# Kernel optimization log

Measured on AMD Instinct MI355X. Metric: run time of the kernel, lower is better.

## Reference

```python
import jax, jax.numpy as jnp
import numpy as np
import math

DIM = 512
HEADS = 8
DIM_HEAD = 64
SCALE = math.sqrt(DIM_HEAD)
EPS = 1e-12


def rms_norm(x, g):
    # F.normalize(x, dim=1) * g * sqrt(dim); x: [B, C, H, W], g: [C]
    inv = jax.lax.rsqrt(jnp.sum(x * x, axis=1, keepdims=True) + EPS)
    return x * inv * g[None, :, None, None] * jnp.asarray(math.sqrt(x.shape[1]), x.dtype)


def setup_inputs() -> dict:
    key = jax.random.key(0)
    k1, k2, k3 = jax.random.split(key, 3)
    B, H, W = 8, 64, 64
    hidden = HEADS * DIM_HEAD
    x = jax.random.normal(k1, (B, DIM, H, W), dtype=jnp.float32)
    w_qkv = jax.random.normal(k2, (3 * hidden, DIM), dtype=jnp.float32) * (1.0 / math.sqrt(DIM))
    w_out = jax.random.normal(k3, (DIM, hidden), dtype=jnp.float32) * (1.0 / math.sqrt(hidden))
    b_out = jnp.zeros((DIM,), dtype=jnp.float32)
    g1 = jnp.ones((DIM,), dtype=jnp.float32)
    g2 = jnp.ones((DIM,), dtype=jnp.float32)
    return {"x": x, "g1": g1, "w_qkv": w_qkv, "w_out": w_out, "b_out": b_out, "g2": g2}


def reference(x, g1, w_qkv, w_out, b_out, g2):
    B, C, H, W = x.shape
    n = H * W
    xn = rms_norm(x, g1)
    # 1x1 conv == channel matmul: [B, 3*hidden, H, W]
    qkv = jnp.einsum('bchw,oc->bohw', xn, w_qkv)
    q, k, v = jnp.split(qkv, 3, axis=1)
    # b (h c) x y -> b h c n
    def to_heads(t):
        return t.reshape(B, HEADS, DIM_HEAD, n)
    q, k, v = to_heads(q), to_heads(k), to_heads(v)
    q = jax.nn.softmax(q, axis=2) / SCALE   # softmax over channel dim d
    k = jax.nn.softmax(k, axis=3)           # softmax over spatial dim n
    context = jnp.einsum('bhdn,bhen->bhde', k, v)   # [B, H, d, e]
    out = jnp.einsum('bhde,bhdn->bhen', context, q) # [B, H, e, n]
    out = out.reshape(B, HEADS * DIM_HEAD, H, W)
    out = jnp.einsum('bchw,oc->bohw', out, w_out) + b_out[None, :, None, None]
    return rms_norm(out, g2)
```

## Files before the change

kernel.cpp:

```cpp
#include <hip/hip_runtime.h>


typedef unsigned short u16;
typedef __attribute__((ext_vector_type(8))) short short8;
typedef __attribute__((ext_vector_type(4))) short short4_t;
typedef __attribute__((ext_vector_type(4))) float f32x4;

static constexpr size_t XN_B = (size_t)512 * 4096;
static constexpr size_t KV_B = (size_t)1024 * 4096;
static constexpr float SQRT512 = 22.62741699796952f;

typedef const __attribute__((address_space(1))) unsigned int gu32;
typedef __attribute__((address_space(3))) unsigned int lu32;

__device__ __forceinline__ float b2f(u16 u){
  union { unsigned u; float f; } x; x.u = ((unsigned)u) << 16; return x.f;
}
__device__ __forceinline__ u16 f2b(float f){
  union { float f; unsigned u; } x; x.f = f;
  unsigned r = x.u + 0x7FFFu + ((x.u >> 16) & 1u);
  return (u16)(r >> 16);
}
__device__ __forceinline__ void gl16(const u16* g, u16* l){
  __builtin_amdgcn_global_load_lds((gu32*)g, (lu32*)l, 16, 0, 0);
}

__global__ __launch_bounds__(256)
void kprep(const float* __restrict__ wqkv, const float* __restrict__ wout,
           const float* __restrict__ g1, u16* __restrict__ dq, u16* __restrict__ dw,
           const float* __restrict__ x, u16* __restrict__ xnT,
           float* __restrict__ sden){
  __shared__ u16 lt[32][514];
  __shared__ float red[256];
  __shared__ float invs[32];
  int bid = blockIdx.x;
  int t = threadIdx.x;
  if (bid < 1024){
    if (bid < 16) sden[bid * 256 + t] = 0.f;
    size_t i = ((size_t)bid * 256 + t) * 4;
    short4_t o;
    if (i < (size_t)786432){
      f32x4 v = *(const f32x4*)(wqkv + i);
      int c = (int)(i & 511);
      #pragma unroll
      for (int j = 0; j < 4; j++) o[j] = (short)f2b(v[j] * g1[c + j] * SQRT512);
      *(short4_t*)(dq + i) = o;
    } else {
      size_t off = i - 786432;
      f32x4 v = *(const f32x4*)(wout + off);
      #pragma unroll
      for (int j = 0; j < 4; j++) o[j] = (short)f2b(v[j]);
      *(short4_t*)(dw + off) = o;
    }
    return;
  }
  int pg0 = (bid - 1024) * 32;
  int b = pg0 >> 12, p0 = pg0 & 4095;
  int px = t & 31, chunk = t >> 5;
  const float* xp = x + (size_t)b * XN_B + p0 + px;
  float s = 0.f;
  #pragma unroll 4
  for (int c = chunk * 64; c < chunk * 64 + 64; ++c){
    float v = xp[(size_t)c * 4096];
    lt[px][c] = f2b(v);
    s += v * v;
  }
  red[t] = s;
  __syncthreads();
  if (chunk == 0){
    float tt = red[px] + red[px + 32] + red[px + 64] + red[px + 96]
             + red[px + 128] + red[px + 160] + red[px + 192] + red[px + 224];
    invs[px] = rsqrtf(tt + 1e-12f);
  }
  __syncthreads();
  int px2 = t >> 3, c0 = (t & 7) * 8;
  float iv = invs[px2];
  u16* dst = xnT + (size_t)(pg0 + px2) * 512;
  #pragma unroll
  for (int j = 0; j < 8; j++){
    int c = c0 + j * 64;
    short8 o;
    #pragma unroll
    for (int e = 0; e < 8; e++) o[e] = (short)f2b(b2f(lt[px2][c + e]) * iv);
    *(short8*)(dst + c) = o;
  }
}

template<int ADD_BIAS, int SMAX>
__global__ __launch_bounds__(512)
void gemm_big(const u16* __restrict__ Ab, long astr, int lda,
              const u16* __restrict__ Bb, long bstr, int ldb,
              u16* __restrict__ Cb, long cstr, int ldc,
              const float* __restrict__ bias)
{
  constexpr int NT = 16;
  const u16* A  = Ab + (size_t)blockIdx.z * astr;
  const u16* BT = Bb + (size_t)blockIdx.z * bstr;
  u16* C = Cb + (size_t)blockIdx.z * cstr;
  const int m0 = blockIdx.y * 256, n0 = blockIdx.x * 256;
  __shared__ u16 As[2][256 * 32];
  __shared__ u16 Bs[2][256 * 32];
  const int tid = threadIdx.x;
  const int lane = tid & 63, wid = tid >> 6;
  const int wr = (wid >> 2) * 128, wc = (wid & 3) * 64;
  const int fr = lane & 15, fq = lane >> 4;
  const int srow = tid >> 2;
  const int sslot = tid & 3;
  f32x4 acc[8][4] = {};

  auto STAGE = [&](int s, int t){
    const int k0 = t * 32;
    #pragma unroll
    for (int r = 0; r < 2; r++){
      int row = r * 128 + srow;
      int gj = (sslot ^ ((row >> 1) & 3)) * 8;
      gl16(A  + (size_t)(m0 + row) * lda + k0 + gj, &As[s][0] + r * 4096 + tid * 8);
      gl16(BT + (size_t)(n0 + row) * ldb + k0 + gj, &Bs[s][0] + r * 4096 + tid * 8);
    }
  };

  STAGE(0, 0);
  int cur = 0;
  for (int t = 0; t < NT; t++){
    if (t + 1 < NT){
      STAGE(cur ^ 1, t + 1);
      asm volatile("s_waitcnt vmcnt(4)" ::: "memory");
    } else {
      asm volatile("s_waitcnt vmcnt(0)" ::: "memory");
    }
    __builtin_amdgcn_s_barrier();
    __builtin_amdgcn_sched_barrier(0);
    short8 a[8], b[4];
    #pragma unroll
    for (int i = 0; i < 8; i++){
      int ra = wr + i * 16 + fr;
      a[i] = *(const short8*)(&As[cur][0] + ra * 32 + ((fq ^ ((ra >> 1) & 3)) * 8));
    }
    #pragma unroll
    for (int j = 0; j < 4; j++){
      int rb = wc + j * 16 + fr;
      b[j] = *(const short8*)(&Bs[cur][0] + rb * 32 + ((fq ^ ((rb >> 1) & 3)) * 8));
    }
    __builtin_amdgcn_s_setprio(1);
    #pragma unroll
    for (int i = 0; i < 8; i++)
      #pragma unroll
      for (int j = 0; j < 4; j++)
        acc[i][j] = __builtin_amdgcn_mfma_f32_16x16x32_bf16(a[i], b[j], acc[i][j], 0, 0, 0);
    __builtin_amdgcn_s_setprio(0);
    __builtin_amdgcn_sched_barrier(0);
    __builtin_amdgcn_s_barrier();
    cur ^= 1;
  }

  if constexpr (SMAX){
    #pragma unroll
    for (int i = 0; i < 8; i++)
      #pragma unroll
      for (int e = 0; e < 4; e++){
        float mx = fmaxf(fmaxf(acc[i][0][e], acc[i][1][e]),
                         fmaxf(acc[i][2][e], acc[i][3][e]));
        mx = fmaxf(mx, __shfl_xor(mx, 1));
        mx = fmaxf(mx, __shfl_xor(mx, 2));
        mx = fmaxf(mx, __shfl_xor(mx, 4));
        mx = fmaxf(mx, __shfl_xor(mx, 8));
        float p0 = __expf(acc[i][0][e] - mx);
        float p1 = __expf(acc[i][1][e] - mx);
        float p2 = __expf(acc[i][2][e] - mx);
        float p3 = __expf(acc[i][3][e] - mx);
        float s = p0 + p1 + p2 + p3;
        s += __shfl_xor(s, 1);
        s += __shfl_xor(s, 2);
        s += __shfl_xor(s, 4);
        s += __shfl_xor(s, 8);
        float r = 1.f / (s * 8.0f);
        acc[i][0][e] = p0 * r; acc[i][1][e] = p1 * r;
        acc[i][2][e] = p2 * r; acc[i][3][e] = p3 * r;
      }
  }
  #pragma unroll
  for (int i = 0; i < 8; i++)
    #pragma unroll
    for (int j = 0; j < 4; j++)
      #pragma unroll
      for (int e = 0; e < 4; e++){
        int row = m0 + wr + i * 16 + fq * 4 + e;
        int col = n0 + wc + j * 16 + fr;
        float v = acc[i][j][e];
        if constexpr (ADD_BIAS) v += bias[col];
        C[(size_t)row * ldc + col] = f2b(v);
      }
}

__global__ __launch_bounds__(256)
void gemm_kv(const u16* __restrict__ Wkv, const u16* __restrict__ xnT,
             u16* __restrict__ kvb)
{
  constexpr int NT = 8;
  const int z = blockIdx.z;
  const u16* A  = Wkv;
  const u16* BT = xnT + (size_t)z * XN_B;
  u16* C = kvb + (size_t)z * KV_B;
  const int m0 = blockIdx.y * 128, n0 = blockIdx.x * 128;
  __shared__ u16 As[2][128 * 64];
  __shared__ u16 Bs[2][128 * 64];
  const int tid = threadIdx.x;
  const int srow0 = tid >> 3;
  const int schunk = tid & 7;
  const int lane = tid & 63, wid = tid >> 6;
  const int wr = (wid >> 1) * 64, wc = (wid & 1) * 64;
  const int fr = lane & 15, fq = lane >> 4;
  f32x4 acc[4][4] = {};

  auto STAGE = [&](int s, int t){
    const int k0 = t * 64;
    #pragma unroll
    for (int r = 0; r < 4; r++){
      int row = r * 32 + srow0;
      int gj = (schunk ^ (row & 7)) * 8;
      gl16(A  + (size_t)(m0 + row) * 512 + k0 + gj, &As[s][0] + r * 2048 + tid * 8);
      gl16(BT + (size_t)(n0 + row) * 512 + k0 + gj, &Bs[s][0] + r * 2048 + tid * 8);
    }
  };

  STAGE(0, 0);
  int cur = 0;
  for (int t = 0; t < NT; t++){
    if (t + 1 < NT){
      STAGE(cur ^ 1, t + 1);
      asm volatile("s_waitcnt vmcnt(8)" ::: "memory");
    } else {
      asm volatile("s_waitcnt vmcnt(0)" ::: "memory");
    }
    __builtin_amdgcn_s_barrier();
    __builtin_amdgcn_sched_barrier(0);
    #pragma unroll
    for (int ks = 0; ks < 2; ks++){
      short8 a[4], b[4];
      #pragma unroll
      for (int i = 0; i < 4; i++){
        int ra = wr + i * 16 + fr;
        a[i] = *(const short8*)(&As[cur][0] + ra * 64 + ((ks * 4 + fq) ^ (ra & 7)) * 8);
        int rb = wc + i * 16 + fr;
        b[i] = *(const short8*)(&Bs[cur][0] + rb * 64 + ((ks * 4 + fq) ^ (rb & 7)) * 8);
      }
      #pragma unroll
      for (int i = 0; i < 4; i++)
        #pragma unroll
        for (int j = 0; j < 4; j++)
          acc[i][j] = __builtin_amdgcn_mfma_f32_16x16x32_bf16(a[i], b[j], acc[i][j], 0, 0, 0);
    }
    __builtin_amdgcn_sched_barrier(0);
    __builtin_amdgcn_s_barrier();
    cur ^= 1;
  }

  #pragma unroll
  for (int i = 0; i < 4; i++)
    #pragma unroll
    for (int j = 0; j < 4; j++)
      #pragma unroll
      for (int e = 0; e < 4; e++){
        int row = m0 + wr + i * 16 + fq * 4 + e;
        int col = n0 + wc + j * 16 + fr;
        C[(size_t)row * 4096 + col] = f2b(acc[i][j][e]);
      }
}

__global__ __launch_bounds__(256)
void gemm_ctx(const u16* __restrict__ kv, float* __restrict__ P,
              float* __restrict__ sden)
{
  constexpr int K = 512;
  const int z = blockIdx.z;
  const int tid = threadIdx.x;
  const int ar = tid >> 2, ac = (tid & 3) * 8;
  int bh = z >> 3, sp = z & 7, b = bh >> 3, h = bh & 7;
  const u16* A  = kv + (size_t)b * KV_B + (size_t)(h * 64) * 4096 + sp * 512;
  const u16* BT = kv + (size_t)b * KV_B + (size_t)(512 + h * 64) * 4096 + sp * 512;
  __shared__ u16 As[64 * 40];
  __shared__ u16 Bs[64 * 40];
  const int wid = tid >> 6, lane = tid & 63;
  const int wr = (wid >> 1) * 32, wc = (wid & 1) * 32;
  const int lr = lane & 15, kb = lane >> 4;
  f32x4 acc[2][2] = {};
  float ssum = 0.f;
  for (int k0 = 0; k0 < K; k0 += 32){
    short8 av = *(const short8*)(A + (size_t)ar * 4096 + k0 + ac);
    short8 ao;
    #pragma unroll
    for (int e = 0; e < 8; e++){
      float ev = __expf(b2f((u16)av[e]));
      ao[e] = (short)f2b(ev);
      ssum += ev;
    }
    *(short8*)(As + ar * 40 + ac) = ao;
    *(short8*)(Bs + ar * 40 + ac) = *(const short8*)(BT + (size_t)ar * 4096 + k0 + ac);
    __syncthreads();
    short8 a0 = *(const short8*)(As + (wr +      lr) * 40 + kb * 8);
    short8 a1 = *(const short8*)(As + (wr + 16 + lr) * 40 + kb * 8);
    short8 b0 = *(const short8*)(Bs + (wc +      lr) * 40 + kb * 8);
    short8 b1 = *(const short8*)(Bs + (wc + 16 + lr) * 40 + kb * 8);
    acc[0][0] = __builtin_amdgcn_mfma_f32_16x16x32_bf16(a0, b0, acc[0][0], 0, 0, 0);
    acc[0][1] = __builtin_amdgcn_mfma_f32_16x16x32_bf16(a0, b1, acc[0][1], 0, 0, 0);
    acc[1][0] = __builtin_amdgcn_mfma_f32_16x16x32_bf16(a1, b0, acc[1][0], 0, 0, 0);
    acc[1][1] = __builtin_amdgcn_mfma_f32_16x16x32_bf16(a1, b1, acc[1][1], 0, 0, 0);
    __syncthreads();
  }
  ssum += __shfl_xor(ssum, 1);
  ssum += __shfl_xor(ssum, 2);
  if ((tid & 3) == 0) atomicAdd(sden + b * 512 + h * 64 + ar, ssum);
  #pragma unroll
  for (int mi = 0; mi < 2; mi++)
    #pragma unroll
    for (int ni = 0; ni < 2; ni++)
      #pragma unroll
      for (int j = 0; j < 4; j++){
        int row = wr + mi * 16 + kb * 4 + j;
        int col = wc + ni * 16 + lr;
        P[(size_t)z * 4096 + (size_t)row * 64 + col] = acc[mi][ni][j];
      }
}

__global__ __launch_bounds__(256)
void kctxw(const float* __restrict__ P, const float* __restrict__ sden,
           const u16* __restrict__ woutbf, u16* __restrict__ M)
{
  const int z = blockIdx.z;
  const int b = z >> 3, h = z & 7;
  const int m0 = blockIdx.y * 64;
  const int tid = threadIdx.x;
  __shared__ u16 As[64 * 72];
  __shared__ u16 Bs[64 * 72];
  {
    int r = tid >> 2, c0 = (tid & 3) * 16;
    const u16* wsrc = woutbf + (size_t)(m0 + r) * 512 + h * 64 + c0;
    *(short8*)(As + r * 72 + c0)     = *(const short8*)(wsrc);
    *(short8*)(As + r * 72 + c0 + 8) = *(const short8*)(wsrc + 8);
    float rs = 1.f / sden[b * 512 + h * 64 + r];
    const float* p = P + (size_t)z * 32768 + (size_t)r * 64 + c0;
    #pragma unroll
    for (int e = 0; e < 16; e++){
      float s = 0.f;
      #pragma unroll
      for (int sp = 0; sp < 8; sp++) s += p[e + sp * 4096];
      Bs[r * 72 + c0 + e] = f2b(s * rs);
    }
  }
  __syncthreads();
  const int wid = tid >> 6, lane = tid & 63;
  const int wr = (wid >> 1) * 32, wc = (wid & 1) * 32;
  const int lr = lane & 15, kb = lane >> 4;
  f32x4 acc[2][2] = {};
  #pragma unroll
  for (int k0 = 0; k0 < 64; k0 += 32){
    short8 a0 = *(const short8*)(As + (wr +      lr) * 72 + k0 + kb * 8);
    short8 a1 = *(const short8*)(As + (wr + 16 + lr) * 72 + k0 + kb * 8);
    short8 b0 = *(const short8*)(Bs + (wc +      lr) * 72 + k0 + kb * 8);
    short8 b1 = *(const short8*)(Bs + (wc + 16 + lr) * 72 + k0 + kb * 8);
    acc[0][0] = __builtin_amdgcn_mfma_f32_16x16x32_bf16(a0, b0, acc[0][0], 0, 0, 0);
    acc[0][1] = __builtin_amdgcn_mfma_f32_16x16x32_bf16(a0, b1, acc[0][1], 0, 0, 0);
    acc[1][0] = __builtin_amdgcn_mfma_f32_16x16x32_bf16(a1, b0, acc[1][0], 0, 0, 0);
    acc[1][1] = __builtin_amdgcn_mfma_f32_16x16x32_bf16(a1, b1, acc[1][1], 0, 0, 0);
  }
  #pragma unroll
  for (int mi = 0; mi < 2; mi++)
    #pragma unroll
    for (int ni = 0; ni < 2; ni++)
      #pragma unroll
      for (int j = 0; j < 4; j++){
        int row = m0 + wr + mi * 16 + kb * 4 + j;
        int col = wc + ni * 16 + lr;
        M[(size_t)b * 262144 + (size_t)row * 512 + h * 64 + col] = f2b(acc[mi][ni][j]);
      }
}

__global__ __launch_bounds__(256)
void krms2(const u16* __restrict__ o2, const float* __restrict__ g,
           float* __restrict__ out){
  __shared__ u16 lt[32][514];
  __shared__ float invs[32];
  __shared__ float gl[512];
  int t = threadIdx.x;
  int pg0 = blockIdx.x * 32;
  int b = pg0 >> 12, p0 = pg0 & 4095;
  gl[t] = g[t] * SQRT512;
  gl[t + 256] = g[t + 256] * SQRT512;
  int px2 = t >> 3, c0 = (t & 7) * 8;
  const u16* src = o2 + (size_t)(pg0 + px2) * 512;
  float s = 0.f;
  #pragma unroll
  for (int j = 0; j < 8; j++){
    int c = c0 + j * 64;
    short8 v = *(const short8*)(src + c);
    *(short8*)&lt[px2][c] = v;
    #pragma unroll
    for (int e = 0; e < 8; e++){ float f = b2f((u16)v[e]); s += f * f; }
  }
  s += __shfl_xor(s, 1); s += __shfl_xor(s, 2); s += __shfl_xor(s, 4);
  if ((t & 7) == 0) invs[px2] = rsqrtf(s + 1e-12f);
  __syncthreads();
  int c2 = t >> 2, pxc = (t & 3) * 8;
  float ivv[8];
  #pragma unroll
  for (int e = 0; e < 8; e++) ivv[e] = invs[pxc + e];
  #pragma unroll
  for (int pass = 0; pass < 8; pass++){
    int c = c2 + pass * 64;
    float gf = gl[c];
    float* dst = out + ((size_t)(b * 512 + c)) * 4096 + p0 + pxc;
    #pragma unroll
    for (int q = 0; q < 2; q++){
      f32x4 o;
      #pragma unroll
      for (int e = 0; e < 4; e++){
        int pp = q * 4 + e;
        o[e] = b2f(lt[pxc + pp][c]) * ivv[pp] * gf;
      }
      *(f32x4*)(dst + q * 4) = o;
    }
  }
}

extern "C" void kernel_launch(void* const* d_in, const int* in_sizes, int n_in,
                              void* d_out, int out_size, void* d_ws, size_t ws_size,
                              hipStream_t stream)
{
  (void)in_sizes; (void)n_in; (void)out_size; (void)ws_size;
  const float* x    = (const float*)d_in[0];
  const float* g1   = (const float*)d_in[1];
  const float* wqkv = (const float*)d_in[2];
  const float* wout = (const float*)d_in[3];
  const float* bout = (const float*)d_in[4];
  const float* g2   = (const float*)d_in[5];
  float* out = (float*)d_out;
  char* ws = (char*)d_ws;

  u16*   xnT   = (u16*)(ws);
  float* P     = (float*)(ws);
  u16*   M     = (u16*)(ws + (size_t)8388608);
  u16*   qT    = (u16*)(ws + (size_t)33554432);
  u16*   kv    = (u16*)(ws + (size_t)67108864);
  u16*   out2T = (u16*)(ws + (size_t)67108864);
  u16*   wbf   = (u16*)(ws + (size_t)134217728);
  u16*   wkvbf = wbf + (size_t)512 * 512;
  u16*   woutbf= (u16*)(ws + (size_t)135790592);
  float* sden  = (float*)(ws + (size_t)136314880);

  kprep<<<2048, 256, 0, stream>>>(wqkv, wout, g1, wbf, woutbf, x, xnT, sden);
  gemm_big<0, 1><<<dim3(2, 128, 1), 512, 0, stream>>>(xnT, 0, 512, wbf, 0, 512,
                                                      qT, 0, 512, nullptr);
  gemm_kv<<<dim3(32, 8, 8), 256, 0, stream>>>(wkvbf, xnT, kv);
  gemm_ctx<<<dim3(1, 1, 512), 256, 0, stream>>>(kv, P, sden);
  kctxw<<<dim3(1, 8, 64), 256, 0, stream>>>(P, sden, woutbf, M);
  gemm_big<1, 0><<<dim3(2, 16, 8), 512, 0, stream>>>(qT, (long)4096 * 512, 512,
                                                     M, (long)262144, 512,
                                                     out2T, (long)4096 * 512, 512, bout);
  krms2<<<1024, 256, 0, stream>>>(out2T, g2, out);
}
```

Measured before the change: 184.3 us.

## Merge Q and KV projection GEMMs into one launch, retile output GEMM to 128x128

```diff
diff --git a/kernel.cpp b/kernel.cpp
--- a/kernel.cpp
+++ b/kernel.cpp
@@ -86,36 +86,43 @@
   }
 }
 
-template<int ADD_BIAS, int SMAX>
-__global__ __launch_bounds__(512)
-void gemm_big(const u16* __restrict__ Ab, long astr, int lda,
-              const u16* __restrict__ Bb, long bstr, int ldb,
-              u16* __restrict__ Cb, long cstr, int ldc,
-              const float* __restrict__ bias)
+__global__ __launch_bounds__(256)
+void gemm_qkv(const u16* __restrict__ Wkv, const u16* __restrict__ wq,
+              const u16* __restrict__ xnT, u16* __restrict__ kvb,
+              u16* __restrict__ qT)
 {
-  constexpr int NT = 16;
-  const u16* A  = Ab + (size_t)blockIdx.z * astr;
-  const u16* BT = Bb + (size_t)blockIdx.z * bstr;
-  u16* C = Cb + (size_t)blockIdx.z * cstr;
-  const int m0 = blockIdx.y * 256, n0 = blockIdx.x * 256;
-  __shared__ u16 As[2][256 * 32];
-  __shared__ u16 Bs[2][256 * 32];
+  constexpr int NT = 8;
+  const int bid = blockIdx.x;
+  const u16* A; const u16* BT; u16* C;
+  int m0, n0; size_t ldc; bool smax;
+  if (bid < 2048){
+    int ntile = bid & 31, mtile = (bid >> 5) & 7, z = bid >> 8;
+    A = Wkv; BT = xnT + (size_t)z * XN_B; C = kvb + (size_t)z * KV_B;
+    m0 = mtile * 128; n0 = ntile * 128; ldc = 4096; smax = false;
+  } else {
+    int idx = bid - 2048;
+    int ntile = idx & 3, mtile = idx >> 2;
+    A = xnT; BT = wq; C = qT;
+    m0 = mtile * 128; n0 = ntile * 128; ldc = 512; smax = true;
+  }
+  __shared__ u16 As[2][128 * 64];
+  __shared__ u16 Bs[2][128 * 64];
   const int tid = threadIdx.x;
+  const int srow0 = tid >> 3;
+  const int schunk = tid & 7;
   const int lane = tid & 63, wid = tid >> 6;
-  const int wr = (wid >> 2) * 128, wc = (wid & 3) * 64;
+  const int wr = (wid >> 1) * 64, wc = (wid & 1) * 64;
   const int fr = lane & 15, fq = lane >> 4;
-  const int srow = tid >> 2;
-  const int sslot = tid & 3;
-  f32x4 acc[8][4] = {};
+  f32x4 acc[4][4] = {};
 
   auto STAGE = [&](int s, int t){
-    const int k0 = t * 32;
-    #pragma unroll
-    for (int r = 0; r < 2; r++){
-      int row = r * 128 + srow;
-      int gj = (sslot ^ ((row >> 1) & 3)) * 8;
-      gl16(A  + (size_t)(m0 + row) * lda + k0 + gj, &As[s][0] + r * 4096 + tid * 8);
-      gl16(BT + (size_t)(n0 + row) * ldb + k0 + gj, &Bs[s][0] + r * 4096 + tid * 8);
+    const int k0 = t * 64;
+    #pragma unroll
+    for (int r = 0; r < 4; r++){
+      int row = r * 32 + srow0;
+      int gj = (schunk ^ (row & 7)) * 8;
+      gl16(A  + (size_t)(m0 + row) * 512 + k0 + gj, &As[s][0] + r * 2048 + tid * 8);
+      gl16(BT + (size_t)(n0 + row) * 512 + k0 + gj, &Bs[s][0] + r * 2048 + tid * 8);
     }
   };
 
@@ -124,38 +131,36 @@
   for (int t = 0; t < NT; t++){
     if (t + 1 < NT){
       STAGE(cur ^ 1, t + 1);
-      asm volatile("s_waitcnt vmcnt(4)" ::: "memory");
+      asm volatile("s_waitcnt vmcnt(8)" ::: "memory");
     } else {
       asm volatile("s_waitcnt vmcnt(0)" ::: "memory");
     }
     __builtin_amdgcn_s_barrier();
     __builtin_amdgcn_sched_barrier(0);
-    short8 a[8], b[4];
-    #pragma unroll
-    for (int i = 0; i < 8; i++){
-      int ra = wr + i * 16 + fr;
-      a[i] = *(const short8*)(&As[cur][0] + ra * 32 + ((fq ^ ((ra >> 1) & 3)) * 8));
-    }
-    #pragma unroll
-    for (int j = 0; j < 4; j++){
-      int rb = wc + j * 16 + fr;
-      b[j] = *(const short8*)(&Bs[cur][0] + rb * 32 + ((fq ^ ((rb >> 1) & 3)) * 8));
-    }
-    __builtin_amdgcn_s_setprio(1);
-    #pragma unroll
-    for (int i = 0; i < 8; i++)
-      #pragma unroll
-      for (int j = 0; j < 4; j++)
-        acc[i][j] = __builtin_amdgcn_mfma_f32_16x16x32_bf16(a[i], b[j], acc[i][j], 0, 0, 0);
-    __builtin_amdgcn_s_setprio(0);
+    #pragma unroll
+    for (int ks = 0; ks < 2; ks++){
+      short8 a[4], b[4];
+      #pragma unroll
+      for (int i = 0; i < 4; i++){
+        int ra = wr + i * 16 + fr;
+        a[i] = *(const short8*)(&As[cur][0] + ra * 64 + ((ks * 4 + fq) ^ (ra & 7)) * 8);
+        int rb = wc + i * 16 + fr;
+        b[i] = *(const short8*)(&Bs[cur][0] + rb * 64 + ((ks * 4 + fq) ^ (rb & 7)) * 8);
+      }
+      #pragma unroll
+      for (int i = 0; i < 4; i++)
+        #pragma unroll
+        for (int j = 0; j < 4; j++)
+          acc[i][j] = __builtin_amdgcn_mfma_f32_16x16x32_bf16(a[i], b[j], acc[i][j], 0, 0, 0);
+    }
     __builtin_amdgcn_sched_barrier(0);
     __builtin_amdgcn_s_barrier();
     cur ^= 1;
   }
 
-  if constexpr (SMAX){
-    #pragma unroll
-    for (int i = 0; i < 8; i++)
+  if (smax){
+    #pragma unroll
+    for (int i = 0; i < 4; i++)
       #pragma unroll
       for (int e = 0; e < 4; e++){
         float mx = fmaxf(fmaxf(acc[i][0][e], acc[i][1][e]),
@@ -179,28 +184,26 @@
       }
   }
   #pragma unroll
-  for (int i = 0; i < 8; i++)
+  for (int i = 0; i < 4; i++)
     #pragma unroll
     for (int j = 0; j < 4; j++)
       #pragma unroll
       for (int e = 0; e < 4; e++){
         int row = m0 + wr + i * 16 + fq * 4 + e;
         int col = n0 + wc + j * 16 + fr;
-        float v = acc[i][j][e];
-        if constexpr (ADD_BIAS) v += bias[col];
-        C[(size_t)row * ldc + col] = f2b(v);
-      }
-}
-
-__global__ __launch_bounds__(256)
-void gemm_kv(const u16* __restrict__ Wkv, const u16* __restrict__ xnT,
-             u16* __restrict__ kvb)
+        C[(size_t)row * ldc + col] = f2b(acc[i][j][e]);
+      }
+}
+
+__global__ __launch_bounds__(256)
+void gemm_out(const u16* __restrict__ qT, const u16* __restrict__ Mb,
+              u16* __restrict__ out2T, const float* __restrict__ bias)
 {
   constexpr int NT = 8;
   const int z = blockIdx.z;
-  const u16* A  = Wkv;
-  const u16* BT = xnT + (size_t)z * XN_B;
-  u16* C = kvb + (size_t)z * KV_B;
+  const u16* A  = qT + (size_t)z * 4096 * 512;
+  const u16* BT = Mb + (size_t)z * 262144;
+  u16* C = out2T + (size_t)z * 4096 * 512;
   const int m0 = blockIdx.y * 128, n0 = blockIdx.x * 128;
   __shared__ u16 As[2][128 * 64];
   __shared__ u16 Bs[2][128 * 64];
@@ -263,7 +266,7 @@
       for (int e = 0; e < 4; e++){
         int row = m0 + wr + i * 16 + fq * 4 + e;
         int col = n0 + wc + j * 16 + fr;
-        C[(size_t)row * 4096 + col] = f2b(acc[i][j][e]);
+        C[(size_t)row * 512 + col] = f2b(acc[i][j][e] + bias[col]);
       }
 }
 
@@ -448,13 +451,9 @@
   float* sden  = (float*)(ws + (size_t)136314880);
 
   kprep<<<2048, 256, 0, stream>>>(wqkv, wout, g1, wbf, woutbf, x, xnT, sden);
-  gemm_big<0, 1><<<dim3(2, 128, 1), 512, 0, stream>>>(xnT, 0, 512, wbf, 0, 512,
-                                                      qT, 0, 512, nullptr);
-  gemm_kv<<<dim3(32, 8, 8), 256, 0, stream>>>(wkvbf, xnT, kv);
+  gemm_qkv<<<3072, 256, 0, stream>>>(wkvbf, wbf, xnT, kv, qT);
   gemm_ctx<<<dim3(1, 1, 512), 256, 0, stream>>>(kv, P, sden);
   kctxw<<<dim3(1, 8, 64), 256, 0, stream>>>(P, sden, woutbf, M);
-  gemm_big<1, 0><<<dim3(2, 16, 8), 512, 0, stream>>>(qT, (long)4096 * 512, 512,
-                                                     M, (long)262144, 512,
-                                                     out2T, (long)4096 * 512, 512, bout);
+  gemm_out<<<dim3(4, 32, 8), 256, 0, stream>>>(qT, M, out2T, bout);
   krms2<<<1024, 256, 0, stream>>>(out2T, g2, out);
 }
```

Measured after the change: 181.5 us. No clear change (-1.6%).
